# Kernel optimization log

Measured on AMD Instinct MI355X. Metric: run time of the kernel, lower is better.

Reference implementation:

```python
import jax, jax.numpy as jnp
import numpy as np

ALPHA, BETA, GAMMA = 1.0, 0.1, 0.1
EPS = 1e-12


def _cubic_kernel(r, h):
    # standard 3D cubic spline kernel
    sigma = 8.0 / (jnp.pi * h ** 3)
    q = r / h
    w = jnp.where(q <= 0.5, 6.0 * (q ** 3 - q ** 2) + 1.0, 2.0 * (1.0 - q) ** 3)
    return sigma * jnp.where(q <= 1.0, w, 0.0)


def _cubic_kernel_dwdr(r, h):
    sigma = 8.0 / (jnp.pi * h ** 3)
    q = r / h
    dw = jnp.where(q <= 0.5, 6.0 * q * (3.0 * q - 2.0), -6.0 * (1.0 - q) ** 2)
    return (sigma / h) * jnp.where(q <= 1.0, dw, 0.0)


def setup_inputs() -> dict:
    key = jax.random.key(0)
    N, NB, D = 6144, 768, 3
    ks = jax.random.split(key, 6)
    mid_pos = jax.random.uniform(ks[0], (N, D), dtype=jnp.float32)  # unit box
    mid_vel = jax.random.normal(ks[1], (N, D), dtype=jnp.float32) * 0.1
    pred = jax.random.normal(ks[2], (N, D), dtype=jnp.float32)
    y = jax.random.normal(ks[3], (N, D), dtype=jnp.float32)
    y_mean = jax.random.normal(ks[4], (D,), dtype=jnp.float32) * 1e-3
    y_std = jax.random.uniform(ks[5], (D,), dtype=jnp.float32) * 2e-3 + 1e-4
    return {
        "pred": pred, "y": y, "mid_pos": mid_pos, "mid_vel": mid_vel,
        "y_mean": y_mean, "y_std": y_std,
        "h": jnp.float32(0.11), "vol": jnp.float32(1.0 / N),
        "rho_0": jnp.float32(1000.0), "dt": jnp.float32(0.005),
        "num_boundary_particles": NB,
    }


def reference(pred, y, mid_pos, mid_vel, y_mean, y_std, h, vol, rho_0, dt,
              num_boundary_particles):
    nb = num_boundary_particles  # static Python int
    # loss1: MSE in standardized space
    loss1 = jnp.mean(jnp.sum((y - pred) ** 2, axis=1))
    # Standardizer.inverse_y
    y_inv = y * y_std + y_mean
    # advect fluid (non-boundary) particles by predicted displacement
    pos = mid_pos.at[nb:].add(y_inv[nb:])
    # radius_graph(pos, h, loop=True) as dense mask over pairwise distances
    sq = jnp.sum(pos * pos, axis=1)  # [N]
    d2 = jnp.maximum(sq[:, None] + sq[None, :] - 2.0 * (pos @ pos.T), 0.0)  # [N,N]
    mask = d2 <= h * h
    r = jnp.sqrt(jnp.maximum(d2, EPS))
    # SPH density: rho_i = rho_0 * vol * sum_j W(r_ij, h)
    W = jnp.where(mask, _cubic_kernel(r, h), 0.0)
    rho = rho_0 * vol * jnp.sum(W, axis=1)
    loss2 = jnp.mean(jnp.abs(rho / rho_0 - 1.0))
    # velocity update for fluid particles
    vel = mid_vel.at[nb:].add(y_inv[nb:] / dt)
    # SPH divergence: div_i = vol * sum_j (v_j - v_i) . gradW_ij,
    # gradW_ij = dW/dr * (x_i - x_j) / r; build the pair dot products via GEMMs:
    # (v_j - v_i).(x_i - x_j) = x_i.v_j + x_j.v_i - x_j.v_j - x_i.v_i
    dwdr = jnp.where(mask, _cubic_kernel_dwdr(r, h), 0.0)
    inv_r = jnp.where(d2 > EPS, 1.0 / r, 0.0)  # self/coincident pairs contribute 0
    Dm = pos @ vel.T  # Dm[i,j] = x_i . v_j
    diag = jnp.sum(pos * vel, axis=1)  # x_k . v_k
    dot = Dm + Dm.T - diag[None, :] - diag[:, None]
    div = vol * jnp.sum(dwdr * inv_r * dot, axis=1)
    loss3 = jnp.mean(jnp.abs(div))
    return ALPHA * loss1 + BETA * loss2 + GAMMA * loss3
```

## Files before the change

kernel.cpp:

```cpp
#include <hip/hip_runtime.h>
#include <math.h>

#define TPB 1024
#define NBLK 243
#define NWAVE (TPB / 64)
#define NCELL 9
#define CAP 1024
#define HCAP 1024
#define PI_F 3.14159265358979323846f
#define EPS_F 1e-12f

__device__ __forceinline__ float wave_reduce(float v) {
#pragma unroll
    for (int off = 32; off > 0; off >>= 1) v += __shfl_down(v, off, 64);
    return v;
}

__device__ __forceinline__ float block_reduce(float v, float* sbuf) {
    v = wave_reduce(v);
    int lane = threadIdx.x & 63;
    int wid  = threadIdx.x >> 6;
    if (lane == 0) sbuf[wid] = v;
    __syncthreads();
    float r = 0.0f;
    if (threadIdx.x == 0) {
        for (int w = 0; w < NWAVE; ++w) r += sbuf[w];
    }
    return r;
}

__device__ __forceinline__ int cell_coord(float x) {
    int c = (int)floorf(x * (float)NCELL);
    return min(max(c, 0), NCELL - 1);
}

__device__ __forceinline__ void pair_math(float xix, float xiy, float xiz,
                                          float vix, float viy, float viz,
                                          float ax, float ay, float az,
                                          float bx, float by, float bz,
                                          float inv_h, float h2,
                                          float& wacc, float& dacc) {
    float dx = xix - ax, dy = xiy - ay, dz = xiz - az;
    float d2 = fmaf(dx, dx, fmaf(dy, dy, dz * dz));
    float r2c = fmaxf(d2, EPS_F);
    float ir  = rsqrtf(r2c);
    float r   = r2c * ir;
    float q   = r * inv_h;
    bool inm = (d2 <= h2) && (q <= 1.0f);
    bool lo  = (q <= 0.5f);
    float q2 = q * q, om = 1.0f - q, om2 = om * om;
    float w  = lo ? fmaf(6.0f, q2 * q - q2, 1.0f) : 2.0f * om2 * om;
    wacc += inm ? w : 0.0f;
    float dw = lo ? q * fmaf(18.0f, q, -12.0f) : -6.0f * om2;
    dw = inm ? dw : 0.0f;
    float irm = (d2 > EPS_F) ? ir : 0.0f;
    float dvx = bx - vix, dvy = by - viy, dvz = bz - viz;
    float dot = fmaf(dvx, dx, fmaf(dvy, dy, dvz * dz));
    dacc = fmaf(dw * irm, dot, dacc);
}

__global__ void __launch_bounds__(TPB) k_main(
    const float* __restrict__ pred, const float* __restrict__ y,
    const float* __restrict__ mid_pos, const float* __restrict__ mid_vel,
    const float* __restrict__ y_mean, const float* __restrict__ y_std,
    const float* __restrict__ h_p, const float* __restrict__ vol_p,
    const float* __restrict__ dt_p, const int* __restrict__ nb_p,
    float* __restrict__ out, int N, float invN)
{
    __shared__ float4 sh4[CAP];
    __shared__ float2 sh2[CAP];
    __shared__ short  s_home[HCAP];
    __shared__ int    s_cnt, s_hcnt;
    __shared__ float  sred[NWAVE];

    int b   = blockIdx.x;
    int tid = threadIdx.x;
    int cx = b / 27, cy = (b / 3) % 9, czg = b % 3;
    int z0 = 3 * czg;

    if (tid == 0) { s_cnt = 0; s_hcnt = 0; }
    __syncthreads();

    int nb = nb_p[0];
    float inv_dt = 1.0f / dt_p[0];
    float ym0 = y_mean[0], ym1 = y_mean[1], ym2 = y_mean[2];
    float ys0 = y_std[0],  ys1 = y_std[1],  ys2 = y_std[2];

    bool do_l1 = (b == 0);
    float t1 = 0.0f;
    int ln = tid & 63;
    unsigned long long lmask = (1ull << ln) - 1ull;

    if (N == TPB * 6) {
        float ppx[6], ppy[6], ppz[6], pvx[6], pvy[6], pvz[6];
        bool inN_[6];
        unsigned long long mN[6];
#pragma unroll
        for (int k = 0; k < 6; ++k) {
            int i = tid + k * TPB;
            float y0 = y[i * 3 + 0], y1 = y[i * 3 + 1], y2 = y[i * 3 + 2];
            float m0 = mid_pos[i * 3 + 0], m1 = mid_pos[i * 3 + 1], m2 = mid_pos[i * 3 + 2];
            float w0 = mid_vel[i * 3 + 0], w1 = mid_vel[i * 3 + 1], w2 = mid_vel[i * 3 + 2];
            if (do_l1) {
                float p0 = pred[i * 3 + 0], p1 = pred[i * 3 + 1], p2 = pred[i * 3 + 2];
                float d0 = y0 - p0, d1 = y1 - p1, d2 = y2 - p2;
                t1 = fmaf(d0, d0, fmaf(d1, d1, fmaf(d2, d2, t1)));
            }
            bool fluid = (i >= nb);
            float i0 = fluid ? fmaf(y0, ys0, ym0) : 0.0f;
            float i1 = fluid ? fmaf(y1, ys1, ym1) : 0.0f;
            float i2 = fluid ? fmaf(y2, ys2, ym2) : 0.0f;
            ppx[k] = m0 + i0; ppy[k] = m1 + i1; ppz[k] = m2 + i2;
            pvx[k] = w0 + i0 * inv_dt; pvy[k] = w1 + i1 * inv_dt; pvz[k] = w2 + i2 * inv_dt;
            int ix = cell_coord(ppx[k]), iy = cell_coord(ppy[k]), iz = cell_coord(ppz[k]);
            inN_[k] = (abs(ix - cx) <= 1) && (abs(iy - cy) <= 1) &&
                      (iz >= z0 - 1) && (iz <= z0 + 3);
            mN[k] = __ballot(inN_[k]);
        }
        int pre[6], tot = 0;
#pragma unroll
        for (int k = 0; k < 6; ++k) { pre[k] = tot; tot += __popcll(mN[k]); }
        int base = 0;
        if (ln == 0 && tot > 0) base = atomicAdd(&s_cnt, tot);
        base = __shfl(base, 0, 64);
#pragma unroll
        for (int k = 0; k < 6; ++k) {
            if (inN_[k]) {
                int slot = base + pre[k] + __popcll(mN[k] & lmask);
                if (slot < CAP) {
                    sh4[slot] = make_float4(ppx[k], ppy[k], ppz[k], pvx[k]);
                    sh2[slot] = make_float2(pvy[k], pvz[k]);
                }
            }
        }
    } else {
        for (int i = tid; i < N; i += TPB) {
            float y0 = y[i * 3 + 0], y1 = y[i * 3 + 1], y2 = y[i * 3 + 2];
            float m0 = mid_pos[i * 3 + 0], m1 = mid_pos[i * 3 + 1], m2 = mid_pos[i * 3 + 2];
            if (do_l1) {
                float p0 = pred[i * 3 + 0], p1 = pred[i * 3 + 1], p2 = pred[i * 3 + 2];
                float d0 = y0 - p0, d1 = y1 - p1, d2 = y2 - p2;
                t1 = fmaf(d0, d0, fmaf(d1, d1, fmaf(d2, d2, t1)));
            }
            bool fluid = (i >= nb);
            float i0 = fluid ? fmaf(y0, ys0, ym0) : 0.0f;
            float i1 = fluid ? fmaf(y1, ys1, ym1) : 0.0f;
            float i2 = fluid ? fmaf(y2, ys2, ym2) : 0.0f;
            float px = m0 + i0, py = m1 + i1, pz = m2 + i2;
            int ix = cell_coord(px), iy = cell_coord(py), iz = cell_coord(pz);
            bool inN = (abs(ix - cx) <= 1) && (abs(iy - cy) <= 1) &&
                       (iz >= z0 - 1) && (iz <= z0 + 3);
            unsigned long long mN = __ballot(inN);
            if (mN) {
                int base = 0;
                if (ln == 0) base = atomicAdd(&s_cnt, __popcll(mN));
                base = __shfl(base, 0, 64);
                if (inN) {
                    int slot = base + __popcll(mN & lmask);
                    if (slot < CAP) {
                        float v0 = mid_vel[i * 3 + 0] + i0 * inv_dt;
                        float v1 = mid_vel[i * 3 + 1] + i1 * inv_dt;
                        float v2 = mid_vel[i * 3 + 2] + i2 * inv_dt;
                        sh4[slot] = make_float4(px, py, pz, v0);
                        sh2[slot] = make_float2(v1, v2);
                    }
                }
            }
        }
    }
    if (do_l1) {
        float s1 = block_reduce(t1, sred);
        if (tid == 0) atomicAdd(out, s1 * invN);
    }
    __syncthreads();

    int T = s_cnt;
    bool staged = (T <= CAP);

    float h = h_p[0], inv_h = 1.0f / h, h2 = h * h;
    float vol = vol_p[0];
    float sigma = 8.0f / (PI_F * h * h * h);
    int wv = tid >> 6;
    float acc = 0.0f;

    if (staged) {
        bool isH = false;
        if (tid < T) {
            float4 a = sh4[tid];
            int ix = cell_coord(a.x), iy = cell_coord(a.y), iz = cell_coord(a.z);
            isH = (ix == cx) && (iy == cy) && (iz >= z0) && (iz <= z0 + 2);
        }
        unsigned long long mH = __ballot(isH);
        if (mH) {
            int hb = 0;
            if (ln == 0) hb = atomicAdd(&s_hcnt, __popcll(mH));
            hb = __shfl(hb, 0, 64);
            if (isH) s_home[hb + __popcll(mH & lmask)] = (short)tid;
        }
        __syncthreads();
        int H = s_hcnt;

        for (int hp = wv; hp < H; hp += NWAVE) {
            int hs = s_home[hp];
            float4 me4 = sh4[hs];
            float2 me2 = sh2[hs];
            float wacc = 0.0f, dacc = 0.0f;
            for (int j = ln; j < T; j += 64) {
                float4 a  = sh4[j];
                float2 b2 = sh2[j];
                pair_math(me4.x, me4.y, me4.z, me4.w, me2.x, me2.y,
                          a.x, a.y, a.z, a.w, b2.x, b2.y, inv_h, h2, wacc, dacc);
            }
            wacc = wave_reduce(wacc);
            dacc = wave_reduce(dacc);
            if (ln == 0) {
                acc += fabsf(fmaf(vol * sigma, wacc, -1.0f))
                     + fabsf(vol * (sigma / h) * dacc);
            }
        }
    } else {
        for (int i = wv; i < N; i += NWAVE) {
            float y0 = y[i * 3 + 0], y1 = y[i * 3 + 1], y2 = y[i * 3 + 2];
            bool fluid = (i >= nb);
            float i0 = fluid ? fmaf(y0, ys0, ym0) : 0.0f;
            float i1 = fluid ? fmaf(y1, ys1, ym1) : 0.0f;
            float i2 = fluid ? fmaf(y2, ys2, ym2) : 0.0f;
            float xix = mid_pos[i * 3 + 0] + i0;
            float xiy = mid_pos[i * 3 + 1] + i1;
            float xiz = mid_pos[i * 3 + 2] + i2;
            int ix = cell_coord(xix), iy = cell_coord(xiy), iz = cell_coord(xiz);
            bool isH = (ix == cx) && (iy == cy) && (iz >= z0) && (iz <= z0 + 2);
            if (!isH) continue;
            float vix = mid_vel[i * 3 + 0] + i0 * inv_dt;
            float viy = mid_vel[i * 3 + 1] + i1 * inv_dt;
            float viz = mid_vel[i * 3 + 2] + i2 * inv_dt;
            float wacc = 0.0f, dacc = 0.0f;
            for (int j = ln; j < N; j += 64) {
                float jy0 = y[j * 3 + 0], jy1 = y[j * 3 + 1], jy2 = y[j * 3 + 2];
                bool jf = (j >= nb);
                float j0 = jf ? fmaf(jy0, ys0, ym0) : 0.0f;
                float j1 = jf ? fmaf(jy1, ys1, ym1) : 0.0f;
                float j2 = jf ? fmaf(jy2, ys2, ym2) : 0.0f;
                float ax = mid_pos[j * 3 + 0] + j0;
                float ay = mid_pos[j * 3 + 1] + j1;
                float az = mid_pos[j * 3 + 2] + j2;
                float bx = mid_vel[j * 3 + 0] + j0 * inv_dt;
                float by = mid_vel[j * 3 + 1] + j1 * inv_dt;
                float bz = mid_vel[j * 3 + 2] + j2 * inv_dt;
                pair_math(xix, xiy, xiz, vix, viy, viz,
                          ax, ay, az, bx, by, bz, inv_h, h2, wacc, dacc);
            }
            wacc = wave_reduce(wacc);
            dacc = wave_reduce(dacc);
            if (ln == 0) {
                acc += fabsf(fmaf(vol * sigma, wacc, -1.0f))
                     + fabsf(vol * (sigma / h) * dacc);
            }
        }
        __syncthreads();
    }

    float tot = block_reduce(acc, sred);
    if (tid == 0) atomicAdd(out, 0.1f * invN * tot);
}

extern "C" void kernel_launch(void* const* d_in, const int* in_sizes, int n_in,
                              void* d_out, int out_size, void* d_ws, size_t ws_size,
                              hipStream_t stream) {
    const float* pred    = (const float*)d_in[0];
    const float* y       = (const float*)d_in[1];
    const float* mid_pos = (const float*)d_in[2];
    const float* mid_vel = (const float*)d_in[3];
    const float* y_mean  = (const float*)d_in[4];
    const float* y_std   = (const float*)d_in[5];
    const float* h_p     = (const float*)d_in[6];
    const float* vol_p   = (const float*)d_in[7];
    const float* dt_p    = (const float*)d_in[9];
    const int*   nb_p    = (const int*)d_in[10];

    int N = in_sizes[0] / 3;
    float invN = 1.0f / (float)N;

    hipMemsetAsync(d_out, 0, sizeof(float), stream);

    k_main<<<NBLK, TPB, 0, stream>>>(pred, y, mid_pos, mid_vel, y_mean, y_std,
                                     h_p, vol_p, dt_p, nb_p,
                                     (float*)d_out, N, invN);
}
```

Baseline: 19.94 us.

## Use one 8x8x8 cell per block and load velocities only for staged particles

Switches the spatial decomposition from 9x9x3 column groups to a full 8x8x8 grid with one home cell per block. This halves per-block home work and shrinks the neighbor halo from 3x3x5 to 3x3x3 cells. Velocity loads and the velocity update are now done only for particles that land in the block's neighborhood, which reduces register pressure and global loads. The tradeoff is more blocks, each scanning the full particle array, and larger cells relative to h.

```diff
diff --git a/kernel.cpp b/kernel.cpp
--- a/kernel.cpp
+++ b/kernel.cpp
@@ -2,9 +2,9 @@
 #include <math.h>
 
 #define TPB 1024
-#define NBLK 243
+#define NCELL 8
+#define NBLK (NCELL * NCELL * NCELL)
 #define NWAVE (TPB / 64)
-#define NCELL 9
 #define CAP 1024
 #define HCAP 1024
 #define PI_F 3.14159265358979323846f
@@ -59,7 +59,7 @@
     dacc = fmaf(dw * irm, dot, dacc);
 }
 
-__global__ void __launch_bounds__(TPB) k_main(
+__global__ void __launch_bounds__(TPB, 8) k_main(
     const float* __restrict__ pred, const float* __restrict__ y,
     const float* __restrict__ mid_pos, const float* __restrict__ mid_vel,
     const float* __restrict__ y_mean, const float* __restrict__ y_std,
@@ -75,8 +75,7 @@
 
     int b   = blockIdx.x;
     int tid = threadIdx.x;
-    int cx = b / 27, cy = (b / 3) % 9, czg = b % 3;
-    int z0 = 3 * czg;
+    int cx = b / (NCELL * NCELL), cy = (b / NCELL) % NCELL, cz = b % NCELL;
 
     if (tid == 0) { s_cnt = 0; s_hcnt = 0; }
     __syncthreads();
@@ -92,7 +91,7 @@
     unsigned long long lmask = (1ull << ln) - 1ull;
 
     if (N == TPB * 6) {
-        float ppx[6], ppy[6], ppz[6], pvx[6], pvy[6], pvz[6];
+        float ppx[6], ppy[6], ppz[6];
         bool inN_[6];
         unsigned long long mN[6];
 #pragma unroll
@@ -100,7 +99,6 @@
             int i = tid + k * TPB;
             float y0 = y[i * 3 + 0], y1 = y[i * 3 + 1], y2 = y[i * 3 + 2];
             float m0 = mid_pos[i * 3 + 0], m1 = mid_pos[i * 3 + 1], m2 = mid_pos[i * 3 + 2];
-            float w0 = mid_vel[i * 3 + 0], w1 = mid_vel[i * 3 + 1], w2 = mid_vel[i * 3 + 2];
             if (do_l1) {
                 float p0 = pred[i * 3 + 0], p1 = pred[i * 3 + 1], p2 = pred[i * 3 + 2];
                 float d0 = y0 - p0, d1 = y1 - p1, d2 = y2 - p2;
@@ -111,10 +109,8 @@
             float i1 = fluid ? fmaf(y1, ys1, ym1) : 0.0f;
             float i2 = fluid ? fmaf(y2, ys2, ym2) : 0.0f;
             ppx[k] = m0 + i0; ppy[k] = m1 + i1; ppz[k] = m2 + i2;
-            pvx[k] = w0 + i0 * inv_dt; pvy[k] = w1 + i1 * inv_dt; pvz[k] = w2 + i2 * inv_dt;
             int ix = cell_coord(ppx[k]), iy = cell_coord(ppy[k]), iz = cell_coord(ppz[k]);
-            inN_[k] = (abs(ix - cx) <= 1) && (abs(iy - cy) <= 1) &&
-                      (iz >= z0 - 1) && (iz <= z0 + 3);
+            inN_[k] = (abs(ix - cx) <= 1) && (abs(iy - cy) <= 1) && (abs(iz - cz) <= 1);
             mN[k] = __ballot(inN_[k]);
         }
         int pre[6], tot = 0;
@@ -128,8 +124,17 @@
             if (inN_[k]) {
                 int slot = base + pre[k] + __popcll(mN[k] & lmask);
                 if (slot < CAP) {
-                    sh4[slot] = make_float4(ppx[k], ppy[k], ppz[k], pvx[k]);
-                    sh2[slot] = make_float2(pvy[k], pvz[k]);
+                    int i = tid + k * TPB;
+                    float y0 = y[i * 3 + 0], y1 = y[i * 3 + 1], y2 = y[i * 3 + 2];
+                    bool fluid = (i >= nb);
+                    float i0 = fluid ? fmaf(y0, ys0, ym0) : 0.0f;
+                    float i1 = fluid ? fmaf(y1, ys1, ym1) : 0.0f;
+                    float i2 = fluid ? fmaf(y2, ys2, ym2) : 0.0f;
+                    float v0 = mid_vel[i * 3 + 0] + i0 * inv_dt;
+                    float v1 = mid_vel[i * 3 + 1] + i1 * inv_dt;
+                    float v2 = mid_vel[i * 3 + 2] + i2 * inv_dt;
+                    sh4[slot] = make_float4(ppx[k], ppy[k], ppz[k], v0);
+                    sh2[slot] = make_float2(v1, v2);
                 }
             }
         }
@@ -148,8 +153,7 @@
             float i2 = fluid ? fmaf(y2, ys2, ym2) : 0.0f;
             float px = m0 + i0, py = m1 + i1, pz = m2 + i2;
             int ix = cell_coord(px), iy = cell_coord(py), iz = cell_coord(pz);
-            bool inN = (abs(ix - cx) <= 1) && (abs(iy - cy) <= 1) &&
-                       (iz >= z0 - 1) && (iz <= z0 + 3);
+            bool inN = (abs(ix - cx) <= 1) && (abs(iy - cy) <= 1) && (abs(iz - cz) <= 1);
             unsigned long long mN = __ballot(inN);
             if (mN) {
                 int base = 0;
@@ -187,8 +191,8 @@
         bool isH = false;
         if (tid < T) {
             float4 a = sh4[tid];
-            int ix = cell_coord(a.x), iy = cell_coord(a.y), iz = cell_coord(a.z);
-            isH = (ix == cx) && (iy == cy) && (iz >= z0) && (iz <= z0 + 2);
+            isH = (cell_coord(a.x) == cx) && (cell_coord(a.y) == cy) &&
+                  (cell_coord(a.z) == cz);
         }
         unsigned long long mH = __ballot(isH);
         if (mH) {
@@ -228,8 +232,8 @@
             float xix = mid_pos[i * 3 + 0] + i0;
             float xiy = mid_pos[i * 3 + 1] + i1;
             float xiz = mid_pos[i * 3 + 2] + i2;
-            int ix = cell_coord(xix), iy = cell_coord(xiy), iz = cell_coord(xiz);
-            bool isH = (ix == cx) && (iy == cy) && (iz >= z0) && (iz <= z0 + 2);
+            bool isH = (cell_coord(xix) == cx) && (cell_coord(xiy) == cy) &&
+                       (cell_coord(xiz) == cz);
             if (!isH) continue;
             float vix = mid_vel[i * 3 + 0] + i0 * inv_dt;
             float viy = mid_vel[i * 3 + 1] + i1 * inv_dt;
```

New measurement: 22.77 us. 14.2% more time.

## Distribute MSE loss across blocks and replace atomics with two-pass reduction

Applied to the files above, without the earlier changes.

The MSE term, previously computed entirely by block 0, is now split so each block handles a small slice. This removes the load imbalance where one block read all of pred. The staging path now loads velocities only for particles that land in the neighbourhood, which cuts register pressure and global loads. The memset and float atomics are replaced by per-block partial sums in workspace plus a second tiny kernel that reduces them, at the cost of an extra launch.

```diff
diff --git a/kernel.cpp b/kernel.cpp
--- a/kernel.cpp
+++ b/kernel.cpp
@@ -16,6 +16,7 @@
     return v;
 }
 
+template<int NT>
 __device__ __forceinline__ float block_reduce(float v, float* sbuf) {
     v = wave_reduce(v);
     int lane = threadIdx.x & 63;
@@ -24,7 +25,7 @@
     __syncthreads();
     float r = 0.0f;
     if (threadIdx.x == 0) {
-        for (int w = 0; w < NWAVE; ++w) r += sbuf[w];
+        for (int w = 0; w < NT / 64; ++w) r += sbuf[w];
     }
     return r;
 }
@@ -65,7 +66,7 @@
     const float* __restrict__ y_mean, const float* __restrict__ y_std,
     const float* __restrict__ h_p, const float* __restrict__ vol_p,
     const float* __restrict__ dt_p, const int* __restrict__ nb_p,
-    float* __restrict__ out, int N, float invN)
+    float* __restrict__ part2, int N, float invN)
 {
     __shared__ float4 sh4[CAP];
     __shared__ float2 sh2[CAP];
@@ -86,13 +87,23 @@
     float ym0 = y_mean[0], ym1 = y_mean[1], ym2 = y_mean[2];
     float ys0 = y_std[0],  ys1 = y_std[1],  ys2 = y_std[2];
 
-    bool do_l1 = (b == 0);
-    float t1 = 0.0f;
     int ln = tid & 63;
     unsigned long long lmask = (1ull << ln) - 1ull;
 
+    int SL = (N + NBLK - 1) / NBLK;
+    float l1t = 0.0f;
+    {
+        int i1 = b * SL + tid;
+        if (tid < SL && i1 < N) {
+            float e0 = y[i1 * 3 + 0] - pred[i1 * 3 + 0];
+            float e1 = y[i1 * 3 + 1] - pred[i1 * 3 + 1];
+            float e2 = y[i1 * 3 + 2] - pred[i1 * 3 + 2];
+            l1t = fmaf(e0, e0, fmaf(e1, e1, e2 * e2));
+        }
+    }
+
     if (N == TPB * 6) {
-        float ppx[6], ppy[6], ppz[6], pvx[6], pvy[6], pvz[6];
+        float ppx[6], ppy[6], ppz[6];
         bool inN_[6];
         unsigned long long mN[6];
 #pragma unroll
@@ -100,18 +111,11 @@
             int i = tid + k * TPB;
             float y0 = y[i * 3 + 0], y1 = y[i * 3 + 1], y2 = y[i * 3 + 2];
             float m0 = mid_pos[i * 3 + 0], m1 = mid_pos[i * 3 + 1], m2 = mid_pos[i * 3 + 2];
-            float w0 = mid_vel[i * 3 + 0], w1 = mid_vel[i * 3 + 1], w2 = mid_vel[i * 3 + 2];
-            if (do_l1) {
-                float p0 = pred[i * 3 + 0], p1 = pred[i * 3 + 1], p2 = pred[i * 3 + 2];
-                float d0 = y0 - p0, d1 = y1 - p1, d2 = y2 - p2;
-                t1 = fmaf(d0, d0, fmaf(d1, d1, fmaf(d2, d2, t1)));
-            }
             bool fluid = (i >= nb);
             float i0 = fluid ? fmaf(y0, ys0, ym0) : 0.0f;
             float i1 = fluid ? fmaf(y1, ys1, ym1) : 0.0f;
             float i2 = fluid ? fmaf(y2, ys2, ym2) : 0.0f;
             ppx[k] = m0 + i0; ppy[k] = m1 + i1; ppz[k] = m2 + i2;
-            pvx[k] = w0 + i0 * inv_dt; pvy[k] = w1 + i1 * inv_dt; pvz[k] = w2 + i2 * inv_dt;
             int ix = cell_coord(ppx[k]), iy = cell_coord(ppy[k]), iz = cell_coord(ppz[k]);
             inN_[k] = (abs(ix - cx) <= 1) && (abs(iy - cy) <= 1) &&
                       (iz >= z0 - 1) && (iz <= z0 + 3);
@@ -128,8 +132,17 @@
             if (inN_[k]) {
                 int slot = base + pre[k] + __popcll(mN[k] & lmask);
                 if (slot < CAP) {
-                    sh4[slot] = make_float4(ppx[k], ppy[k], ppz[k], pvx[k]);
-                    sh2[slot] = make_float2(pvy[k], pvz[k]);
+                    int i = tid + k * TPB;
+                    float y0 = y[i * 3 + 0], y1 = y[i * 3 + 1], y2 = y[i * 3 + 2];
+                    bool fluid = (i >= nb);
+                    float i0 = fluid ? fmaf(y0, ys0, ym0) : 0.0f;
+                    float i1 = fluid ? fmaf(y1, ys1, ym1) : 0.0f;
+                    float i2 = fluid ? fmaf(y2, ys2, ym2) : 0.0f;
+                    float v0 = mid_vel[i * 3 + 0] + i0 * inv_dt;
+                    float v1 = mid_vel[i * 3 + 1] + i1 * inv_dt;
+                    float v2 = mid_vel[i * 3 + 2] + i2 * inv_dt;
+                    sh4[slot] = make_float4(ppx[k], ppy[k], ppz[k], v0);
+                    sh2[slot] = make_float2(v1, v2);
                 }
             }
         }
@@ -137,11 +150,6 @@
         for (int i = tid; i < N; i += TPB) {
             float y0 = y[i * 3 + 0], y1 = y[i * 3 + 1], y2 = y[i * 3 + 2];
             float m0 = mid_pos[i * 3 + 0], m1 = mid_pos[i * 3 + 1], m2 = mid_pos[i * 3 + 2];
-            if (do_l1) {
-                float p0 = pred[i * 3 + 0], p1 = pred[i * 3 + 1], p2 = pred[i * 3 + 2];
-                float d0 = y0 - p0, d1 = y1 - p1, d2 = y2 - p2;
-                t1 = fmaf(d0, d0, fmaf(d1, d1, fmaf(d2, d2, t1)));
-            }
             bool fluid = (i >= nb);
             float i0 = fluid ? fmaf(y0, ys0, ym0) : 0.0f;
             float i1 = fluid ? fmaf(y1, ys1, ym1) : 0.0f;
@@ -167,10 +175,6 @@
                 }
             }
         }
-    }
-    if (do_l1) {
-        float s1 = block_reduce(t1, sred);
-        if (tid == 0) atomicAdd(out, s1 * invN);
     }
     __syncthreads();
 
@@ -260,8 +264,19 @@
         __syncthreads();
     }
 
-    float tot = block_reduce(acc, sred);
-    if (tid == 0) atomicAdd(out, 0.1f * invN * tot);
+    float v = acc * (0.1f * invN) + l1t * invN;
+    float tot = block_reduce<TPB>(v, sred);
+    if (tid == 0) part2[b] = tot;
+}
+
+__global__ void __launch_bounds__(256) k_final(
+    const float* __restrict__ part2, float* __restrict__ out)
+{
+    __shared__ float sred[256 / 64];
+    float s = 0.0f;
+    for (int k = threadIdx.x; k < NBLK; k += 256) s += part2[k];
+    float tot = block_reduce<256>(s, sred);
+    if (threadIdx.x == 0) out[0] = tot;
 }
 
 extern "C" void kernel_launch(void* const* d_in, const int* in_sizes, int n_in,
@@ -281,9 +296,10 @@
     int N = in_sizes[0] / 3;
     float invN = 1.0f / (float)N;
 
-    hipMemsetAsync(d_out, 0, sizeof(float), stream);
+    float* part2 = (float*)d_ws;
 
     k_main<<<NBLK, TPB, 0, stream>>>(pred, y, mid_pos, mid_vel, y_mean, y_std,
-                                     h_p, vol_p, dt_p, nb_p,
-                                     (float*)d_out, N, invN);
-}
+                                     h_p, vol_p, dt_p, nb_p, part2, N, invN);
+
+    k_final<<<1, 256, 0, stream>>>(part2, (float*)d_out);
+}
```

New measurement: 17.08 us (median of 2 runs). -14.4%, faster.
